# Performance work log

Hardware: AMD Instinct MI355X
Metric: run time of the kernel (lower is better)

## Reference

```python
import jax, jax.numpy as jnp
import numpy as np

NUM_GRAPHS = 128
NODES_PER_GRAPH = 512
NUM_NODES = NUM_GRAPHS * NODES_PER_GRAPH
NUM_EDGES = NUM_NODES * 16
IN_DIM = 64
HID = 128
NUM_HEADS = 4
BN_EPS = 1e-5


def setup_inputs() -> dict:
    key = jax.random.key(0)
    ks = jax.random.split(key, 12)
    x = jax.random.normal(ks[0], (NUM_NODES, IN_DIM), dtype=jnp.float32)
    edge_index = jax.random.randint(ks[1], (2, NUM_EDGES), 0, NUM_NODES, dtype=jnp.int32)
    batch = jnp.repeat(jnp.arange(NUM_GRAPHS, dtype=jnp.int32), NODES_PER_GRAPH)
    s = 0.05
    W0 = jax.random.normal(ks[2], (IN_DIM, HID), dtype=jnp.float32) * s
    b0 = jnp.zeros((HID,), jnp.float32)
    Wh = jax.random.normal(ks[3], (3, HID, HID), dtype=jnp.float32) * s  # convs 1..3
    bh = jnp.zeros((3, HID), jnp.float32)
    bn_gamma = jnp.ones((4, HID), jnp.float32)
    bn_beta = jnp.zeros((4, HID), jnp.float32)
    bn_mean = jnp.zeros((4, HID), jnp.float32)
    bn_var = jnp.ones((4, HID), jnp.float32)
    attn_in_w = jax.random.normal(ks[4], (3 * HID, HID), dtype=jnp.float32) * s
    attn_in_b = jnp.zeros((3 * HID,), jnp.float32)
    attn_out_w = jax.random.normal(ks[5], (HID, HID), dtype=jnp.float32) * s
    attn_out_b = jnp.zeros((HID,), jnp.float32)
    return dict(x=x, W0=W0, b0=b0, Wh=Wh, bh=bh, bn_gamma=bn_gamma, bn_beta=bn_beta,
                bn_mean=bn_mean, bn_var=bn_var, attn_in_w=attn_in_w, attn_in_b=attn_in_b,
                attn_out_w=attn_out_w, attn_out_b=attn_out_b, edge_index=edge_index, batch=batch)


def _forward(x, W0, b0, Wh, bh, bn_gamma, bn_beta, bn_mean, bn_var,
             attn_in_w, attn_in_b, attn_out_w, attn_out_b, edge_index, batch):
    N = x.shape[0]
    src, dst = edge_index[0], edge_index[1]
    # GCN symmetric normalization with self-loops (PyG GCNConv)
    deg = jax.ops.segment_sum(jnp.ones_like(src, jnp.float32), dst, num_segments=N) + 1.0
    dis = jax.lax.rsqrt(deg)                      # deg^{-1/2}
    enorm = (dis[src] * dis[dst])[:, None]        # per-edge norm
    self_norm = (dis * dis)[:, None]              # self-loop norm

    def gcn(h, W, b):
        h = h @ W
        agg = jax.ops.segment_sum(h[src] * enorm, dst, num_segments=N)
        return agg + h * self_norm + b

    def bn(h, i):
        scale = bn_gamma[i] * jax.lax.rsqrt(bn_var[i] + BN_EPS)
        return (h - bn_mean[i]) * scale + bn_beta[i]  # eval-mode BN

    # dropout is identity in eval mode
    h = jax.nn.relu(bn(gcn(x, W0, b0), 0))
    h = jax.nn.relu(bn(gcn(h, Wh[0], bh[0]), 1))
    h = jax.nn.relu(bn(gcn(h, Wh[1], bh[1]), 2))
    f = jax.nn.relu(bn(gcn(h, Wh[2], bh[2]), 3))   # [N, HID]

    # per-graph self-attention (equal-size contiguous graphs -> batched MHA)
    dh = HID // NUM_HEADS
    xg = f.reshape(NUM_GRAPHS, NODES_PER_GRAPH, HID)
    qkv = xg @ attn_in_w.T + attn_in_b            # [G, n, 3H]
    q, k, v = jnp.split(qkv, 3, axis=-1)

    def heads(t):
        return t.reshape(NUM_GRAPHS, NODES_PER_GRAPH, NUM_HEADS, dh).transpose(0, 2, 1, 3)
    q, k, v = heads(q), heads(k), heads(v)
    scores = jnp.einsum('ghnd,ghmd->ghnm', q, k) / np.sqrt(dh).astype(np.float32)
    attn = jax.nn.softmax(scores, axis=-1)
    o = jnp.einsum('ghnm,ghmd->ghnd', attn, v).transpose(0, 2, 1, 3).reshape(NUM_GRAPHS, NODES_PER_GRAPH, HID)
    o = o @ attn_out_w.T + attn_out_b
    final = o.reshape(N, HID)

    # global mean pool over batch indices
    cnt = jax.ops.segment_sum(jnp.ones((N,), jnp.float32), batch, num_segments=NUM_GRAPHS)
    graph_emb = jax.ops.segment_sum(final, batch, num_segments=NUM_GRAPHS) / cnt[:, None]
    return final, graph_emb


def reference(x, W0, b0, Wh, bh, bn_gamma, bn_beta, bn_mean, bn_var,
              attn_in_w, attn_in_b, attn_out_w, attn_out_b, edge_index, batch):
    return _forward(x, W0, b0, Wh, bh, bn_gamma, bn_beta, bn_mean, bn_var,
                    attn_in_w, attn_in_b, attn_out_w, attn_out_b, edge_index, batch)
```

## Files before the change

### kernel.cpp

```cpp
#include <hip/hip_runtime.h>
#include <hip/hip_bf16.h>
#include <cstdint>
#include <cstddef>

#define N_NODES 65536
#define N_EDGES 1048576
#define N_GRAPHS 128
#define NPG 512
#define IN_DIM 64
#define HID 128
#define BN_EPS 1e-5f

typedef __attribute__((ext_vector_type(8))) short bf16x8;
typedef __attribute__((ext_vector_type(4))) float f32x4;
typedef __attribute__((ext_vector_type(8))) unsigned short u16x8;
typedef __attribute__((ext_vector_type(4))) unsigned short u16x4;

__device__ inline unsigned short f2bf(float f) {
  unsigned u = __builtin_bit_cast(unsigned, f);
  u = u + 0x7fffu + ((u >> 16) & 1u);
  return (unsigned short)(u >> 16);
}
__device__ inline float bf2f(unsigned short h) {
  unsigned u = ((unsigned)h) << 16;
  return __builtin_bit_cast(float, u);
}
__device__ inline void split_bf(float v, unsigned short& hi, unsigned short& lo) {
  hi = f2bf(v);
  lo = f2bf(v - bf2f(hi));
}
__device__ inline bf16x8 ld_bf8(const unsigned short* p) {
  u16x4 a = *(const u16x4*)p;
  u16x4 b = *(const u16x4*)(p + 4);
  u16x8 r = __builtin_shufflevector(a, b, 0, 1, 2, 3, 4, 5, 6, 7);
  return __builtin_bit_cast(bf16x8, r);
}

__global__ __launch_bounds__(256) void hist_kernel(const int* __restrict__ dst,
                                                   int* __restrict__ deg) {
  int e = blockIdx.x * 256 + threadIdx.x;
  if (e < N_EDGES) atomicAdd(&deg[dst[e]], 1);
}

__global__ __launch_bounds__(256) void dis_kernel(const int* __restrict__ deg,
                                                  float* __restrict__ dis) {
  int n = blockIdx.x * 256 + threadIdx.x;
  if (n < N_NODES) dis[n] = 1.0f / sqrtf((float)deg[n] + 1.0f);
}

__global__ __launch_bounds__(1024) void scan_kernel(const int* __restrict__ deg,
                                                    int* __restrict__ offsets,
                                                    int* __restrict__ cursor) {
  __shared__ int sums[1024];
  int t = threadIdx.x;
  int base = t * 64;
  const int4* dp = (const int4*)(deg + base);
  int s = 0;
#pragma unroll
  for (int i = 0; i < 16; i++) {
    int4 v = dp[i];
    s += v.x + v.y + v.z + v.w;
  }
  sums[t] = s;
  __syncthreads();
  for (int off = 1; off < 1024; off <<= 1) {
    int v = (t >= off) ? sums[t - off] : 0;
    __syncthreads();
    sums[t] += v;
    __syncthreads();
  }
  int run = (t == 0) ? 0 : sums[t - 1];
#pragma unroll
  for (int i = 0; i < 16; i++) {
    int4 v = dp[i];
    int idx = base + i * 4;
    offsets[idx] = run; cursor[idx] = run; run += v.x;
    offsets[idx + 1] = run; cursor[idx + 1] = run; run += v.y;
    offsets[idx + 2] = run; cursor[idx + 2] = run; run += v.z;
    offsets[idx + 3] = run; cursor[idx + 3] = run; run += v.w;
  }
  if (t == 1023) offsets[N_NODES] = run;
}

__global__ __launch_bounds__(256) void fill_kernel(const int* __restrict__ src,
                                                   const int* __restrict__ dst,
                                                   const float* __restrict__ dis,
                                                   int* __restrict__ cursor,
                                                   int* __restrict__ csr,
                                                   float* __restrict__ wedge) {
  int e = blockIdx.x * 256 + threadIdx.x;
  if (e < N_EDGES) {
    int d = dst[e];
    int s = src[e];
    int slot = atomicAdd(&cursor[d], 1);
    csr[slot] = s;
    wedge[slot] = dis[s] * dis[d];
  }
}

__global__ __launch_bounds__(256) void agg64_kernel(const float* __restrict__ x,
                                                    const float* __restrict__ dis,
                                                    const float* __restrict__ wedge,
                                                    const int* __restrict__ offsets,
                                                    const int* __restrict__ csr,
                                                    unsigned short* __restrict__ zhi,
                                                    unsigned short* __restrict__ zlo) {
  int node = blockIdx.x * 4 + (threadIdx.x >> 6);
  int lane = threadIdx.x & 63;
  float dn = dis[node];
  float acc = x[(size_t)node * 64 + lane] * dn * dn;
  int beg = offsets[node], end = offsets[node + 1];
  int k = beg;
  for (; k + 8 <= end; k += 8) {
    int s[8];
    float w[8], v[8];
#pragma unroll
    for (int i = 0; i < 8; i++) {
      s[i] = csr[k + i];
      w[i] = wedge[k + i];
    }
#pragma unroll
    for (int i = 0; i < 8; i++) v[i] = x[(size_t)s[i] * 64 + lane];
#pragma unroll
    for (int i = 0; i < 8; i++) acc = fmaf(w[i], v[i], acc);
  }
  for (; k + 4 <= end; k += 4) {
    int s0 = csr[k], s1 = csr[k + 1], s2 = csr[k + 2], s3 = csr[k + 3];
    float w0 = wedge[k], w1 = wedge[k + 1], w2 = wedge[k + 2], w3 = wedge[k + 3];
    float v0 = x[(size_t)s0 * 64 + lane];
    float v1 = x[(size_t)s1 * 64 + lane];
    float v2 = x[(size_t)s2 * 64 + lane];
    float v3 = x[(size_t)s3 * 64 + lane];
    acc = fmaf(w0, v0, acc);
    acc = fmaf(w1, v1, acc);
    acc = fmaf(w2, v2, acc);
    acc = fmaf(w3, v3, acc);
  }
  for (; k < end; k++) {
    int s = csr[k];
    acc = fmaf(wedge[k], x[(size_t)s * 64 + lane], acc);
  }
  unsigned short h_, l_;
  split_bf(acc, h_, l_);
  zhi[(size_t)node * 64 + lane] = h_;
  zlo[(size_t)node * 64 + lane] = l_;
}

__global__ __launch_bounds__(256) void agg128_kernel(const float* __restrict__ h,
                                                     const float* __restrict__ dis,
                                                     const float* __restrict__ wedge,
                                                     const int* __restrict__ offsets,
                                                     const int* __restrict__ csr,
                                                     unsigned short* __restrict__ zhi,
                                                     unsigned short* __restrict__ zlo) {
  int node = blockIdx.x * 4 + (threadIdx.x >> 6);
  int lane = threadIdx.x & 63;
  float dn = dis[node];
  float sn = dn * dn;
  const float* hr = h + (size_t)node * 128;
  float a0 = hr[lane] * sn;
  float a1 = hr[lane + 64] * sn;
  int beg = offsets[node], end = offsets[node + 1];
  int k = beg;
  for (; k + 8 <= end; k += 8) {
    int s[8];
    float w[8], u[8], d[8];
#pragma unroll
    for (int i = 0; i < 8; i++) {
      s[i] = csr[k + i];
      w[i] = wedge[k + i];
    }
#pragma unroll
    for (int i = 0; i < 8; i++) {
      const float* p = h + (size_t)s[i] * 128;
      u[i] = p[lane];
      d[i] = p[lane + 64];
    }
#pragma unroll
    for (int i = 0; i < 8; i++) {
      a0 = fmaf(w[i], u[i], a0);
      a1 = fmaf(w[i], d[i], a1);
    }
  }
  for (; k + 4 <= end; k += 4) {
    int s0 = csr[k], s1 = csr[k + 1], s2 = csr[k + 2], s3 = csr[k + 3];
    float w0 = wedge[k], w1 = wedge[k + 1], w2 = wedge[k + 2], w3 = wedge[k + 3];
    const float* p0 = h + (size_t)s0 * 128;
    const float* p1 = h + (size_t)s1 * 128;
    const float* p2 = h + (size_t)s2 * 128;
    const float* p3 = h + (size_t)s3 * 128;
    float u0 = p0[lane], d0 = p0[lane + 64];
    float u1 = p1[lane], d1 = p1[lane + 64];
    float u2 = p2[lane], d2 = p2[lane + 64];
    float u3 = p3[lane], d3 = p3[lane + 64];
    a0 = fmaf(w0, u0, a0); a1 = fmaf(w0, d0, a1);
    a0 = fmaf(w1, u1, a0); a1 = fmaf(w1, d1, a1);
    a0 = fmaf(w2, u2, a0); a1 = fmaf(w2, d2, a1);
    a0 = fmaf(w3, u3, a0); a1 = fmaf(w3, d3, a1);
  }
  for (; k < end; k++) {
    int s = csr[k];
    float wt = wedge[k];
    const float* hs = h + (size_t)s * 128;
    a0 = fmaf(wt, hs[lane], a0);
    a1 = fmaf(wt, hs[lane + 64], a1);
  }
  unsigned short h0, l0, h1, l1;
  split_bf(a0, h0, l0);
  split_bf(a1, h1, l1);
  zhi[(size_t)node * 128 + lane] = h0;
  zlo[(size_t)node * 128 + lane] = l0;
  zhi[(size_t)node * 128 + lane + 64] = h1;
  zlo[(size_t)node * 128 + lane + 64] = l1;
}

template <bool TRANS>
__global__ __launch_bounds__(256) void wprep_kernel(const float* __restrict__ W, int K, int O,
                                                    unsigned short* __restrict__ hi,
                                                    unsigned short* __restrict__ lo) {
  int idx = blockIdx.x * 256 + threadIdx.x;
  int KC = K / 32;
  int total = (O / 16) * KC * 64;
  if (idx >= total) return;
  int lane = idx & 63;
  int rest = idx >> 6;
  int kc = rest % KC;
  int nt = rest / KC;
  int n = nt * 16 + (lane & 15);
  int kb = kc * 32 + (lane >> 4) * 8;
  unsigned short* hp = hi + (size_t)idx * 8;
  unsigned short* lp = lo + (size_t)idx * 8;
#pragma unroll
  for (int j = 0; j < 8; j++) {
    int k = kb + j;
    float v = TRANS ? W[(size_t)n * K + k] : W[(size_t)k * O + n];
    unsigned short h_, l_;
    split_bf(v, h_, l_);
    hp[j] = h_;
    lp[j] = l_;
  }
}

template <int K, int O, bool DOBN, bool DORELU, bool SPLIT_OUT>
__global__ __launch_bounds__(256) void gemm_mfma(
    const unsigned short* __restrict__ Ahi, const unsigned short* __restrict__ Alo,
    const unsigned short* __restrict__ Whi, const unsigned short* __restrict__ Wlo,
    const float* __restrict__ bias,
    const float* __restrict__ gamma, const float* __restrict__ beta,
    const float* __restrict__ mean, const float* __restrict__ var,
    float* __restrict__ Cf, unsigned short* __restrict__ Chi,
    unsigned short* __restrict__ Clo) {
  constexpr int KC = K / 32;
  int wave = threadIdx.x >> 6;
  int lane = threadIdx.x & 63;
  int m0 = blockIdx.x * 128 + wave * 32;
  int o0 = blockIdx.y * 128;
  int mrow = lane & 15;
  int kseg = (lane >> 4) * 8;

  f32x4 acc[2][8];
#pragma unroll
  for (int mt = 0; mt < 2; mt++)
#pragma unroll
    for (int nt = 0; nt < 8; nt++) acc[mt][nt] = (f32x4)0.0f;

#pragma unroll
  for (int kc = 0; kc < KC; kc++) {
    bf16x8 ah[2], al[2];
#pragma unroll
    for (int mt = 0; mt < 2; mt++) {
      size_t aoff = (size_t)(m0 + mt * 16 + mrow) * K + kc * 32 + kseg;
      ah[mt] = *(const bf16x8*)(Ahi + aoff);
      al[mt] = *(const bf16x8*)(Alo + aoff);
    }
#pragma unroll
    for (int nt = 0; nt < 8; nt++) {
      size_t foff = (((size_t)(blockIdx.y * 8 + nt) * KC + kc) * 64 + lane) * 8;
      bf16x8 bh = *(const bf16x8*)(Whi + foff);
      bf16x8 bl = *(const bf16x8*)(Wlo + foff);
#pragma unroll
      for (int mt = 0; mt < 2; mt++) {
        acc[mt][nt] = __builtin_amdgcn_mfma_f32_16x16x32_bf16(ah[mt], bh, acc[mt][nt], 0, 0, 0);
        acc[mt][nt] = __builtin_amdgcn_mfma_f32_16x16x32_bf16(ah[mt], bl, acc[mt][nt], 0, 0, 0);
        acc[mt][nt] = __builtin_amdgcn_mfma_f32_16x16x32_bf16(al[mt], bh, acc[mt][nt], 0, 0, 0);
      }
    }
  }

  int ccol = lane & 15;
  int crow0 = (lane >> 4) * 4;
#pragma unroll
  for (int nt = 0; nt < 8; nt++) {
    int c = o0 + nt * 16 + ccol;
    float sc, cb;
    float b = bias[c];
    if (DOBN) {
      sc = gamma[c] * rsqrtf(var[c] + BN_EPS);
      cb = (b - mean[c]) * sc + beta[c];
    } else {
      sc = 1.0f;
      cb = b;
    }
#pragma unroll
    for (int mt = 0; mt < 2; mt++) {
#pragma unroll
      for (int r = 0; r < 4; r++) {
        float v = fmaf(acc[mt][nt][r], sc, cb);
        if (DORELU) v = fmaxf(v, 0.0f);
        size_t row = (size_t)(m0 + mt * 16 + crow0 + r);
        if (SPLIT_OUT) {
          unsigned short h_, l_;
          split_bf(v, h_, l_);
          Chi[row * O + c] = h_;
          Clo[row * O + c] = l_;
        } else {
          Cf[row * O + c] = v;
        }
      }
    }
  }
}

__global__ __launch_bounds__(256) void knorm_kernel(const float* __restrict__ qkv,
                                                    float* __restrict__ kmax2) {
  int g = blockIdx.x >> 2;
  int h = blockIdx.x & 3;
  size_t gbase = (size_t)g * NPG;
  float best = 0.0f;
#pragma unroll
  for (int r = 0; r < 2; r++) {
    int j = r * 256 + threadIdx.x;
    const float* kp = &qkv[(gbase + j) * 384 + 128 + h * 32];
    float s = 0.0f;
#pragma unroll
    for (int i = 0; i < 8; i++) {
      float4 v = *(const float4*)(kp + i * 4);
      s = fmaf(v.x, v.x, s);
      s = fmaf(v.y, v.y, s);
      s = fmaf(v.z, v.z, s);
      s = fmaf(v.w, v.w, s);
    }
    best = fmaxf(best, s);
  }
#pragma unroll
  for (int off = 32; off >= 1; off >>= 1)
    best = fmaxf(best, __shfl_xor(best, off, 64));
  __shared__ float red[4];
  int wave = threadIdx.x >> 6;
  if ((threadIdx.x & 63) == 0) red[wave] = best;
  __syncthreads();
  if (threadIdx.x == 0) {
    float m = fmaxf(fmaxf(red[0], red[1]), fmaxf(red[2], red[3]));
    kmax2[blockIdx.x] = m;
  }
}

__global__ __launch_bounds__(256, 2) void attn_mfma_kernel(
    const float* __restrict__ qkv, const float* __restrict__ kmax2,
    unsigned short* __restrict__ ohi, unsigned short* __restrict__ olo) {
  int b = blockIdx.x;
  int g = b >> 3;
  int h = (b >> 1) & 3;
  int half = b & 1;
  int t = threadIdx.x;
  int wave = t >> 6;
  int lane = t & 63;
  int quad = lane >> 4;
  int l15 = lane & 15;
  size_t gbase = (size_t)g * NPG;
  int qb = half * 256 + wave * 64;

  const float cf = 0.17677669529663687f * 1.4426950408889634f;

  __shared__ unsigned short Kh[32][36], Kl[32][36];
  __shared__ unsigned short Vh[33][36], Vl[33][36];
  __shared__ char wbuf[4][9472] __attribute__((aligned(16)));

  unsigned short* Ph = (unsigned short*)wbuf[wave];
  unsigned short* Pl = Ph + 64 * 36;
  float* Ot = (float*)wbuf[wave];

  bf16x8 qh[4], ql[4];
  float qn2p[4];
#pragma unroll
  for (int mt = 0; mt < 4; mt++) {
    const float* qp = &qkv[(gbase + qb + mt * 16 + l15) * 384 + h * 32 + quad * 8];
    float4 f0 = *(const float4*)qp;
    float4 f1 = *(const float4*)(qp + 4);
    float v[8] = {f0.x * cf, f0.y * cf, f0.z * cf, f0.w * cf,
                  f1.x * cf, f1.y * cf, f1.z * cf, f1.w * cf};
    u16x8 hh, ll;
    float s = 0.0f;
#pragma unroll
    for (int j = 0; j < 8; j++) {
      unsigned short hi_, lo_;
      split_bf(v[j], hi_, lo_);
      hh[j] = hi_;
      ll[j] = lo_;
      s = fmaf(v[j], v[j], s);
    }
    qh[mt] = __builtin_bit_cast(bf16x8, hh);
    ql[mt] = __builtin_bit_cast(bf16x8, ll);
    s += __shfl_xor(s, 16);
    s += __shfl_xor(s, 32);
    qn2p[mt] = s;
  }
  if (quad == 0) {
#pragma unroll
    for (int mt = 0; mt < 4; mt++) Ot[mt * 16 + l15] = qn2p[mt];
  }
  float km2 = kmax2[g * 4 + h];
  float Mq[4][4];
#pragma unroll
  for (int mt = 0; mt < 4; mt++)
#pragma unroll
    for (int r = 0; r < 4; r++)
      Mq[mt][r] = sqrtf(Ot[mt * 16 + quad * 4 + r] * km2);

  f32x4 Oa[4][3];
#pragma unroll
  for (int mt = 0; mt < 4; mt++)
#pragma unroll
    for (int nt = 0; nt < 3; nt++) Oa[mt][nt] = (f32x4)0.0f;

  for (int c = 0; c < 16; c++) {
    __syncthreads();
    if (t >= 128) {
      int t2 = t - 128;
      int key = t2 >> 2;
      int ds = (t2 & 3) * 8;
      const float* kp = &qkv[(gbase + (size_t)(c * 32 + key)) * 384 + 128 + h * 32 + ds];
      float4 f0 = *(const float4*)kp;
      float4 f1 = *(const float4*)(kp + 4);
      float v[8] = {f0.x, f0.y, f0.z, f0.w, f1.x, f1.y, f1.z, f1.w};
      u16x4 h0, h1, l0, l1;
#pragma unroll
      for (int j = 0; j < 4; j++) {
        unsigned short hi_, lo_;
        split_bf(v[j], hi_, lo_);
        h0[j] = hi_; l0[j] = lo_;
        split_bf(v[j + 4], hi_, lo_);
        h1[j] = hi_; l1[j] = lo_;
      }
      *(u16x4*)&Kh[key][ds] = h0;
      *(u16x4*)&Kh[key][ds + 4] = h1;
      *(u16x4*)&Kl[key][ds] = l0;
      *(u16x4*)&Kl[key][ds + 4] = l1;
    } else if (t < 64) {
      int keyb = (t & 7) * 4;
      int dvb = (t >> 3) * 4;
      float4 r0 = *(const float4*)&qkv[(gbase + (size_t)(c * 32 + keyb + 0)) * 384 + 256 + h * 32 + dvb];
      float4 r1 = *(const float4*)&qkv[(gbase + (size_t)(c * 32 + keyb + 1)) * 384 + 256 + h * 32 + dvb];
      float4 r2 = *(const float4*)&qkv[(gbase + (size_t)(c * 32 + keyb + 2)) * 384 + 256 + h * 32 + dvb];
      float4 r3 = *(const float4*)&qkv[(gbase + (size_t)(c * 32 + keyb + 3)) * 384 + 256 + h * 32 + dvb];
      float rr[4][4] = {{r0.x, r0.y, r0.z, r0.w}, {r1.x, r1.y, r1.z, r1.w},
                        {r2.x, r2.y, r2.z, r2.w}, {r3.x, r3.y, r3.z, r3.w}};
#pragma unroll
      for (int c2 = 0; c2 < 4; c2++) {
        ushort4 hv, lv;
        unsigned short hi_, lo_;
        split_bf(rr[0][c2], hi_, lo_); hv.x = hi_; lv.x = lo_;
        split_bf(rr[1][c2], hi_, lo_); hv.y = hi_; lv.y = lo_;
        split_bf(rr[2][c2], hi_, lo_); hv.z = hi_; lv.z = lo_;
        split_bf(rr[3][c2], hi_, lo_); hv.w = hi_; lv.w = lo_;
        *(ushort4*)&Vh[dvb + c2][keyb] = hv;
        *(ushort4*)&Vl[dvb + c2][keyb] = lv;
      }
    } else if (t < 68) {
      int i = t - 64;
      u16x8 ones;
#pragma unroll
      for (int j = 0; j < 8; j++) ones[j] = 0x3F80;
      *(u16x4*)&Vh[32][i * 8] = __builtin_shufflevector(ones, ones, 0, 1, 2, 3);
      *(u16x4*)&Vh[32][i * 8 + 4] = __builtin_shufflevector(ones, ones, 4, 5, 6, 7);
    }
    __syncthreads();

#pragma unroll
    for (int nt = 0; nt < 2; nt++) {
      bf16x8 bkh = ld_bf8(&Kh[nt * 16 + l15][quad * 8]);
      bf16x8 bkl = ld_bf8(&Kl[nt * 16 + l15][quad * 8]);
#pragma unroll
      for (int mt = 0; mt < 4; mt++) {
        f32x4 S = (f32x4)0.0f;
        S = __builtin_amdgcn_mfma_f32_16x16x32_bf16(qh[mt], bkh, S, 0, 0, 0);
        S = __builtin_amdgcn_mfma_f32_16x16x32_bf16(qh[mt], bkl, S, 0, 0, 0);
        S = __builtin_amdgcn_mfma_f32_16x16x32_bf16(ql[mt], bkh, S, 0, 0, 0);
#pragma unroll
        for (int r = 0; r < 4; r++) {
          float p = __builtin_exp2f(S[r] - Mq[mt][r]);
          unsigned short hi_, lo_;
          split_bf(p, hi_, lo_);
          int row = mt * 16 + quad * 4 + r;
          Ph[row * 36 + nt * 16 + l15] = hi_;
          Pl[row * 36 + nt * 16 + l15] = lo_;
        }
      }
    }
    bf16x8 pah[4], pal[4];
#pragma unroll
    for (int mt = 0; mt < 4; mt++) {
      pah[mt] = ld_bf8(&Ph[(mt * 16 + l15) * 36 + quad * 8]);
      pal[mt] = ld_bf8(&Pl[(mt * 16 + l15) * 36 + quad * 8]);
    }
#pragma unroll
    for (int nt = 0; nt < 3; nt++) {
      bf16x8 bvh = ld_bf8(&Vh[nt * 16 + l15][quad * 8]);
      if (nt < 2) {
        bf16x8 bvl = ld_bf8(&Vl[nt * 16 + l15][quad * 8]);
#pragma unroll
        for (int mt = 0; mt < 4; mt++) {
          Oa[mt][nt] = __builtin_amdgcn_mfma_f32_16x16x32_bf16(pah[mt], bvh, Oa[mt][nt], 0, 0, 0);
          Oa[mt][nt] = __builtin_amdgcn_mfma_f32_16x16x32_bf16(pah[mt], bvl, Oa[mt][nt], 0, 0, 0);
          Oa[mt][nt] = __builtin_amdgcn_mfma_f32_16x16x32_bf16(pal[mt], bvh, Oa[mt][nt], 0, 0, 0);
        }
      } else {
#pragma unroll
        for (int mt = 0; mt < 4; mt++) {
          Oa[mt][nt] = __builtin_amdgcn_mfma_f32_16x16x32_bf16(pah[mt], bvh, Oa[mt][nt], 0, 0, 0);
          Oa[mt][nt] = __builtin_amdgcn_mfma_f32_16x16x32_bf16(pal[mt], bvh, Oa[mt][nt], 0, 0, 0);
        }
      }
    }
  }

#pragma unroll
  for (int mt = 0; mt < 4; mt++) {
#pragma unroll
    for (int r = 0; r < 4; r++) {
      int row = mt * 16 + quad * 4 + r;
      Ot[row * 37 + l15] = Oa[mt][0][r];
      Ot[row * 37 + 16 + l15] = Oa[mt][1][r];
      if (l15 == 0) Ot[row * 37 + 32] = Oa[mt][2][r];
    }
  }
  {
    int row = lane;
    float inv = 1.0f / Ot[row * 37 + 32];
    size_t node = gbase + qb + row;
    u16x8 vh, vl;
#pragma unroll
    for (int seg = 0; seg < 4; seg++) {
#pragma unroll
      for (int j = 0; j < 8; j++) {
        unsigned short hi_, lo_;
        split_bf(Ot[row * 37 + seg * 8 + j] * inv, hi_, lo_);
        vh[j] = hi_;
        vl[j] = lo_;
      }
      *(u16x8*)(ohi + node * 128 + h * 32 + seg * 8) = vh;
      *(u16x8*)(olo + node * 128 + h * 32 + seg * 8) = vl;
    }
  }
}

__global__ __launch_bounds__(128) void pool_kernel(const float* __restrict__ fin,
                                                   float* __restrict__ emb) {
  int g = blockIdx.x, c = threadIdx.x;
  const float* p = fin + (size_t)g * NPG * HID + c;
  float s = 0.0f;
  for (int i = 0; i < NPG; i++) s += p[(size_t)i * HID];
  emb[g * HID + c] = s * (1.0f / NPG);
}

extern "C" void kernel_launch(void* const* d_in, const int* in_sizes, int n_in,
                              void* d_out, int out_size, void* d_ws, size_t ws_size,
                              hipStream_t stream) {
  (void)in_sizes; (void)n_in; (void)out_size; (void)ws_size;
  const float* x          = (const float*)d_in[0];
  const float* W0         = (const float*)d_in[1];
  const float* b0         = (const float*)d_in[2];
  const float* Wh         = (const float*)d_in[3];
  const float* bh         = (const float*)d_in[4];
  const float* bn_gamma   = (const float*)d_in[5];
  const float* bn_beta    = (const float*)d_in[6];
  const float* bn_mean    = (const float*)d_in[7];
  const float* bn_var     = (const float*)d_in[8];
  const float* attn_in_w  = (const float*)d_in[9];
  const float* attn_in_b  = (const float*)d_in[10];
  const float* attn_out_w = (const float*)d_in[11];
  const float* attn_out_b = (const float*)d_in[12];
  const int* edge_index   = (const int*)d_in[13];
  const int* src = edge_index;
  const int* dst = edge_index + N_EDGES;

  char* ws = (char*)d_ws;
  size_t off = 0;
  auto alloc = [&](size_t bytes) -> void* {
    void* p = ws + off;
    off += (bytes + 255) & ~(size_t)255;
    return p;
  };
  int*   deg     = (int*)alloc((size_t)N_NODES * 4);
  int*   offsets = (int*)alloc((size_t)(N_NODES + 1) * 4);
  int*   cursor  = (int*)alloc((size_t)N_NODES * 4);
  int*   csr     = (int*)alloc((size_t)N_EDGES * 4);
  float* wedge   = (float*)alloc((size_t)N_EDGES * 4);
  float* dis     = (float*)alloc((size_t)N_NODES * 4);
  float* bufA    = (float*)alloc((size_t)N_NODES * HID * 4);
  unsigned short* zhi = (unsigned short*)alloc((size_t)N_NODES * HID * 2);
  unsigned short* zlo = (unsigned short*)alloc((size_t)N_NODES * HID * 2);
  float* qkvb    = (float*)alloc((size_t)N_NODES * 384 * 4);
  float* kmax2   = (float*)alloc((size_t)N_GRAPHS * 4 * 4);
  unsigned short* w0h = (unsigned short*)alloc(8192 * 2);
  unsigned short* w0l = (unsigned short*)alloc(8192 * 2);
  unsigned short* whh[3], *whl[3];
  for (int i = 0; i < 3; i++) {
    whh[i] = (unsigned short*)alloc(16384 * 2);
    whl[i] = (unsigned short*)alloc(16384 * 2);
  }
  unsigned short* wqh = (unsigned short*)alloc(49152 * 2);
  unsigned short* wql = (unsigned short*)alloc(49152 * 2);
  unsigned short* woh = (unsigned short*)alloc(16384 * 2);
  unsigned short* wol = (unsigned short*)alloc(16384 * 2);

  unsigned short* fhi = (unsigned short*)bufA;
  unsigned short* flo = fhi + (size_t)N_NODES * HID;

  float* fin = (float*)d_out;
  float* emb = fin + (size_t)N_NODES * HID;

  hipMemsetAsync(deg, 0, (size_t)N_NODES * 4, stream);
  hist_kernel<<<N_EDGES / 256, 256, 0, stream>>>(dst, deg);
  dis_kernel<<<N_NODES / 256, 256, 0, stream>>>(deg, dis);
  scan_kernel<<<1, 1024, 0, stream>>>(deg, offsets, cursor);
  fill_kernel<<<N_EDGES / 256, 256, 0, stream>>>(src, dst, dis, cursor, csr, wedge);

  wprep_kernel<false><<<4, 256, 0, stream>>>(W0, 64, 128, w0h, w0l);
  for (int i = 0; i < 3; i++)
    wprep_kernel<false><<<8, 256, 0, stream>>>(Wh + (size_t)i * HID * HID, 128, 128,
                                               whh[i], whl[i]);
  wprep_kernel<true><<<24, 256, 0, stream>>>(attn_in_w, 128, 384, wqh, wql);
  wprep_kernel<true><<<8, 256, 0, stream>>>(attn_out_w, 128, 128, woh, wol);

  dim3 ggrid(N_NODES / 128, 1);
  agg64_kernel<<<N_NODES / 4, 256, 0, stream>>>(x, dis, wedge, offsets, csr, zhi, zlo);
  gemm_mfma<64, 128, true, true, false><<<ggrid, 256, 0, stream>>>(
      zhi, zlo, w0h, w0l, b0, bn_gamma, bn_beta, bn_mean, bn_var, bufA, nullptr, nullptr);
  for (int L = 0; L < 2; L++) {
    agg128_kernel<<<N_NODES / 4, 256, 0, stream>>>(bufA, dis, wedge, offsets, csr, zhi, zlo);
    gemm_mfma<128, 128, true, true, false><<<ggrid, 256, 0, stream>>>(
        zhi, zlo, whh[L], whl[L], bh + (size_t)L * HID,
        bn_gamma + (size_t)(L + 1) * HID, bn_beta + (size_t)(L + 1) * HID,
        bn_mean + (size_t)(L + 1) * HID, bn_var + (size_t)(L + 1) * HID,
        bufA, nullptr, nullptr);
  }
  agg128_kernel<<<N_NODES / 4, 256, 0, stream>>>(bufA, dis, wedge, offsets, csr, zhi, zlo);
  gemm_mfma<128, 128, true, true, true><<<ggrid, 256, 0, stream>>>(
      zhi, zlo, whh[2], whl[2], bh + (size_t)2 * HID,
      bn_gamma + (size_t)3 * HID, bn_beta + (size_t)3 * HID,
      bn_mean + (size_t)3 * HID, bn_var + (size_t)3 * HID,
      nullptr, fhi, flo);
  dim3 qgrid(N_NODES / 128, 3);
  gemm_mfma<128, 384, false, false, false><<<qgrid, 256, 0, stream>>>(
      fhi, flo, wqh, wql, attn_in_b, nullptr, nullptr, nullptr, nullptr,
      qkvb, nullptr, nullptr);
  knorm_kernel<<<N_GRAPHS * 4, 256, 0, stream>>>(qkvb, kmax2);
  attn_mfma_kernel<<<N_GRAPHS * 4 * 2, 256, 0, stream>>>(qkvb, kmax2, zhi, zlo);
  gemm_mfma<128, 128, false, false, false><<<ggrid, 256, 0, stream>>>(
      zhi, zlo, woh, wol, attn_out_b, nullptr, nullptr, nullptr, nullptr,
      fin, nullptr, nullptr);
  pool_kernel<<<N_GRAPHS, 128, 0, stream>>>(fin, emb);
}
```

Before: 841.9 us.

## Store node features in 16-column slabs to make sparse aggregation cache-friendly

```diff
diff --git a/kernel.cpp b/kernel.cpp
--- a/kernel.cpp
+++ b/kernel.cpp
@@ -98,120 +98,65 @@
   }
 }
 
-__global__ __launch_bounds__(256) void agg64_kernel(const float* __restrict__ x,
-                                                    const float* __restrict__ dis,
-                                                    const float* __restrict__ wedge,
-                                                    const int* __restrict__ offsets,
-                                                    const int* __restrict__ csr,
-                                                    unsigned short* __restrict__ zhi,
-                                                    unsigned short* __restrict__ zlo) {
+__global__ __launch_bounds__(256) void xslab_kernel(const float* __restrict__ x,
+                                                    float* __restrict__ xs) {
   int node = blockIdx.x * 4 + (threadIdx.x >> 6);
   int lane = threadIdx.x & 63;
-  float dn = dis[node];
-  float acc = x[(size_t)node * 64 + lane] * dn * dn;
-  int beg = offsets[node], end = offsets[node + 1];
-  int k = beg;
-  for (; k + 8 <= end; k += 8) {
-    int s[8];
-    float w[8], v[8];
-#pragma unroll
-    for (int i = 0; i < 8; i++) {
-      s[i] = csr[k + i];
-      w[i] = wedge[k + i];
-    }
-#pragma unroll
-    for (int i = 0; i < 8; i++) v[i] = x[(size_t)s[i] * 64 + lane];
-#pragma unroll
-    for (int i = 0; i < 8; i++) acc = fmaf(w[i], v[i], acc);
-  }
-  for (; k + 4 <= end; k += 4) {
-    int s0 = csr[k], s1 = csr[k + 1], s2 = csr[k + 2], s3 = csr[k + 3];
-    float w0 = wedge[k], w1 = wedge[k + 1], w2 = wedge[k + 2], w3 = wedge[k + 3];
-    float v0 = x[(size_t)s0 * 64 + lane];
-    float v1 = x[(size_t)s1 * 64 + lane];
-    float v2 = x[(size_t)s2 * 64 + lane];
-    float v3 = x[(size_t)s3 * 64 + lane];
-    acc = fmaf(w0, v0, acc);
-    acc = fmaf(w1, v1, acc);
-    acc = fmaf(w2, v2, acc);
-    acc = fmaf(w3, v3, acc);
-  }
-  for (; k < end; k++) {
-    int s = csr[k];
-    acc = fmaf(wedge[k], x[(size_t)s * 64 + lane], acc);
-  }
-  unsigned short h_, l_;
-  split_bf(acc, h_, l_);
-  zhi[(size_t)node * 64 + lane] = h_;
-  zlo[(size_t)node * 64 + lane] = l_;
-}
-
-__global__ __launch_bounds__(256) void agg128_kernel(const float* __restrict__ h,
-                                                     const float* __restrict__ dis,
-                                                     const float* __restrict__ wedge,
-                                                     const int* __restrict__ offsets,
-                                                     const int* __restrict__ csr,
-                                                     unsigned short* __restrict__ zhi,
-                                                     unsigned short* __restrict__ zlo) {
-  int node = blockIdx.x * 4 + (threadIdx.x >> 6);
+  int s = lane >> 4, d = lane & 15;
+  xs[((size_t)s * N_NODES + node) * 16 + d] = x[(size_t)node * 64 + lane];
+}
+
+template <int NS>
+__global__ __launch_bounds__(256) void agg_slab_kernel(
+    const float* __restrict__ hs, const float* __restrict__ dis,
+    const float* __restrict__ wedge, const int* __restrict__ offsets,
+    const int* __restrict__ csr, unsigned short* __restrict__ zhi,
+    unsigned short* __restrict__ zlo) {
+  int b = blockIdx.x;
+  int s = b & (NS - 1);
+  int grp = b / NS;
+  int w = threadIdx.x >> 6;
   int lane = threadIdx.x & 63;
-  float dn = dis[node];
-  float sn = dn * dn;
-  const float* hr = h + (size_t)node * 128;
-  float a0 = hr[lane] * sn;
-  float a1 = hr[lane + 64] * sn;
-  int beg = offsets[node], end = offsets[node + 1];
-  int k = beg;
-  for (; k + 8 <= end; k += 8) {
-    int s[8];
-    float w[8], u[8], d[8];
-#pragma unroll
-    for (int i = 0; i < 8; i++) {
-      s[i] = csr[k + i];
-      w[i] = wedge[k + i];
-    }
-#pragma unroll
-    for (int i = 0; i < 8; i++) {
-      const float* p = h + (size_t)s[i] * 128;
-      u[i] = p[lane];
-      d[i] = p[lane + 64];
-    }
-#pragma unroll
-    for (int i = 0; i < 8; i++) {
-      a0 = fmaf(w[i], u[i], a0);
-      a1 = fmaf(w[i], d[i], a1);
-    }
-  }
-  for (; k + 4 <= end; k += 4) {
-    int s0 = csr[k], s1 = csr[k + 1], s2 = csr[k + 2], s3 = csr[k + 3];
-    float w0 = wedge[k], w1 = wedge[k + 1], w2 = wedge[k + 2], w3 = wedge[k + 3];
-    const float* p0 = h + (size_t)s0 * 128;
-    const float* p1 = h + (size_t)s1 * 128;
-    const float* p2 = h + (size_t)s2 * 128;
-    const float* p3 = h + (size_t)s3 * 128;
-    float u0 = p0[lane], d0 = p0[lane + 64];
-    float u1 = p1[lane], d1 = p1[lane + 64];
-    float u2 = p2[lane], d2 = p2[lane + 64];
-    float u3 = p3[lane], d3 = p3[lane + 64];
-    a0 = fmaf(w0, u0, a0); a1 = fmaf(w0, d0, a1);
-    a0 = fmaf(w1, u1, a0); a1 = fmaf(w1, d1, a1);
-    a0 = fmaf(w2, u2, a0); a1 = fmaf(w2, d2, a1);
-    a0 = fmaf(w3, u3, a0); a1 = fmaf(w3, d3, a1);
-  }
-  for (; k < end; k++) {
-    int s = csr[k];
-    float wt = wedge[k];
-    const float* hs = h + (size_t)s * 128;
-    a0 = fmaf(wt, hs[lane], a0);
-    a1 = fmaf(wt, hs[lane + 64], a1);
-  }
-  unsigned short h0, l0, h1, l1;
-  split_bf(a0, h0, l0);
-  split_bf(a1, h1, l1);
-  zhi[(size_t)node * 128 + lane] = h0;
-  zlo[(size_t)node * 128 + lane] = l0;
-  zhi[(size_t)node * 128 + lane + 64] = h1;
-  zlo[(size_t)node * 128 + lane + 64] = l1;
+  int e = lane >> 4, d = lane & 15;
+  const float* slab = hs + (size_t)s * N_NODES * 16;
+  const int OD = NS * 16;
+#pragma unroll 1
+  for (int i = 0; i < 4; i++) {
+    int node = (grp * 4 + w) * 4 + i;
+    int beg = offsets[node], end = offsets[node + 1];
+    float acc = 0.0f;
+    int k = beg;
+    for (; k + 8 <= end; k += 8) {
+      int i0 = csr[k + e], i1 = csr[k + 4 + e];
+      float w0 = wedge[k + e], w1 = wedge[k + 4 + e];
+      float v0 = slab[(size_t)i0 * 16 + d];
+      float v1 = slab[(size_t)i1 * 16 + d];
+      acc = fmaf(w0, v0, acc);
+      acc = fmaf(w1, v1, acc);
+    }
+    if (k + 4 <= end) {
+      int i0 = csr[k + e];
+      float w0 = wedge[k + e];
+      acc = fmaf(w0, slab[(size_t)i0 * 16 + d], acc);
+      k += 4;
+    }
+    int rem = end - k;
+    if (rem > 0) {
+      int i0 = (e < rem) ? csr[k + e] : 0;
+      float w0 = (e < rem) ? wedge[k + e] : 0.0f;
+      acc = fmaf(w0, slab[(size_t)i0 * 16 + d], acc);
+    }
+    acc += __shfl_xor(acc, 16);
+    acc += __shfl_xor(acc, 32);
+    if (e == 0) {
+      float dn = dis[node];
+      float v = fmaf(slab[(size_t)node * 16 + d], dn * dn, acc);
+      unsigned short h_, l_;
+      split_bf(v, h_, l_);
+      zhi[(size_t)node * OD + s * 16 + d] = h_;
+      zlo[(size_t)node * OD + s * 16 + d] = l_;
+    }
+  }
 }
 
 template <bool TRANS>
@@ -241,7 +186,7 @@
   }
 }
 
-template <int K, int O, bool DOBN, bool DORELU, bool SPLIT_OUT>
+template <int K, int O, bool DOBN, bool DORELU, int OUTMODE>
 __global__ __launch_bounds__(256) void gemm_mfma(
     const unsigned short* __restrict__ Ahi, const unsigned short* __restrict__ Alo,
     const unsigned short* __restrict__ Whi, const unsigned short* __restrict__ Wlo,
@@ -308,11 +253,13 @@
         float v = fmaf(acc[mt][nt][r], sc, cb);
         if (DORELU) v = fmaxf(v, 0.0f);
         size_t row = (size_t)(m0 + mt * 16 + crow0 + r);
-        if (SPLIT_OUT) {
+        if (OUTMODE == 1) {
           unsigned short h_, l_;
           split_bf(v, h_, l_);
           Chi[row * O + c] = h_;
           Clo[row * O + c] = l_;
+        } else if (OUTMODE == 2) {
+          Cf[((size_t)(c >> 4) * N_NODES + row) * 16 + (c & 15)] = v;
         } else {
           Cf[row * O + c] = v;
         }
@@ -597,7 +544,8 @@
   int*   csr     = (int*)alloc((size_t)N_EDGES * 4);
   float* wedge   = (float*)alloc((size_t)N_EDGES * 4);
   float* dis     = (float*)alloc((size_t)N_NODES * 4);
-  float* bufA    = (float*)alloc((size_t)N_NODES * HID * 4);
+  float* hsl     = (float*)alloc((size_t)N_NODES * HID * 4);
+  float* xs      = (float*)alloc((size_t)N_NODES * 64 * 4);
   unsigned short* zhi = (unsigned short*)alloc((size_t)N_NODES * HID * 2);
   unsigned short* zlo = (unsigned short*)alloc((size_t)N_NODES * HID * 2);
   float* qkvb    = (float*)alloc((size_t)N_NODES * 384 * 4);
@@ -614,7 +562,7 @@
   unsigned short* woh = (unsigned short*)alloc(16384 * 2);
   unsigned short* wol = (unsigned short*)alloc(16384 * 2);
 
-  unsigned short* fhi = (unsigned short*)bufA;
+  unsigned short* fhi = (unsigned short*)hsl;
   unsigned short* flo = fhi + (size_t)N_NODES * HID;
 
   float* fin = (float*)d_out;
@@ -633,31 +581,36 @@
   wprep_kernel<true><<<24, 256, 0, stream>>>(attn_in_w, 128, 384, wqh, wql);
   wprep_kernel<true><<<8, 256, 0, stream>>>(attn_out_w, 128, 128, woh, wol);
 
+  xslab_kernel<<<N_NODES / 4, 256, 0, stream>>>(x, xs);
+
   dim3 ggrid(N_NODES / 128, 1);
-  agg64_kernel<<<N_NODES / 4, 256, 0, stream>>>(x, dis, wedge, offsets, csr, zhi, zlo);
-  gemm_mfma<64, 128, true, true, false><<<ggrid, 256, 0, stream>>>(
-      zhi, zlo, w0h, w0l, b0, bn_gamma, bn_beta, bn_mean, bn_var, bufA, nullptr, nullptr);
+  agg_slab_kernel<4><<<(N_NODES / 16) * 4, 256, 0, stream>>>(
+      xs, dis, wedge, offsets, csr, zhi, zlo);
+  gemm_mfma<64, 128, true, true, 2><<<ggrid, 256, 0, stream>>>(
+      zhi, zlo, w0h, w0l, b0, bn_gamma, bn_beta, bn_mean, bn_var, hsl, nullptr, nullptr);
   for (int L = 0; L < 2; L++) {
-    agg128_kernel<<<N_NODES / 4, 256, 0, stream>>>(bufA, dis, wedge, offsets, csr, zhi, zlo);
-    gemm_mfma<128, 128, true, true, false><<<ggrid, 256, 0, stream>>>(
+    agg_slab_kernel<8><<<(N_NODES / 16) * 8, 256, 0, stream>>>(
+        hsl, dis, wedge, offsets, csr, zhi, zlo);
+    gemm_mfma<128, 128, true, true, 2><<<ggrid, 256, 0, stream>>>(
         zhi, zlo, whh[L], whl[L], bh + (size_t)L * HID,
         bn_gamma + (size_t)(L + 1) * HID, bn_beta + (size_t)(L + 1) * HID,
         bn_mean + (size_t)(L + 1) * HID, bn_var + (size_t)(L + 1) * HID,
-        bufA, nullptr, nullptr);
-  }
-  agg128_kernel<<<N_NODES / 4, 256, 0, stream>>>(bufA, dis, wedge, offsets, csr, zhi, zlo);
-  gemm_mfma<128, 128, true, true, true><<<ggrid, 256, 0, stream>>>(
+        hsl, nullptr, nullptr);
+  }
+  agg_slab_kernel<8><<<(N_NODES / 16) * 8, 256, 0, stream>>>(
+      hsl, dis, wedge, offsets, csr, zhi, zlo);
+  gemm_mfma<128, 128, true, true, 1><<<ggrid, 256, 0, stream>>>(
       zhi, zlo, whh[2], whl[2], bh + (size_t)2 * HID,
       bn_gamma + (size_t)3 * HID, bn_beta + (size_t)3 * HID,
       bn_mean + (size_t)3 * HID, bn_var + (size_t)3 * HID,
       nullptr, fhi, flo);
   dim3 qgrid(N_NODES / 128, 3);
-  gemm_mfma<128, 384, false, false, false><<<qgrid, 256, 0, stream>>>(
+  gemm_mfma<128, 384, false, false, 0><<<qgrid, 256, 0, stream>>>(
       fhi, flo, wqh, wql, attn_in_b, nullptr, nullptr, nullptr, nullptr,
       qkvb, nullptr, nullptr);
   knorm_kernel<<<N_GRAPHS * 4, 256, 0, stream>>>(qkvb, kmax2);
   attn_mfma_kernel<<<N_GRAPHS * 4 * 2, 256, 0, stream>>>(qkvb, kmax2, zhi, zlo);
-  gemm_mfma<128, 128, false, false, false><<<ggrid, 256, 0, stream>>>(
+  gemm_mfma<128, 128, false, false, 0><<<ggrid, 256, 0, stream>>>(
       zhi, zlo, woh, wol, attn_out_b, nullptr, nullptr, nullptr, nullptr,
       fin, nullptr, nullptr);
   pool_kernel<<<N_GRAPHS, 128, 0, stream>>>(fin, emb);
```

Result: slower. 1.230 ms (+46.1%).

## Fuse GCN neighbor aggregation into the MFMA GEMM with an LDS-staged tile

Applied to the files above, without the earlier changes.

```diff
diff --git a/kernel.cpp b/kernel.cpp
--- a/kernel.cpp
+++ b/kernel.cpp
@@ -96,122 +96,6 @@
     csr[slot] = s;
     wedge[slot] = dis[s] * dis[d];
   }
-}
-
-__global__ __launch_bounds__(256) void agg64_kernel(const float* __restrict__ x,
-                                                    const float* __restrict__ dis,
-                                                    const float* __restrict__ wedge,
-                                                    const int* __restrict__ offsets,
-                                                    const int* __restrict__ csr,
-                                                    unsigned short* __restrict__ zhi,
-                                                    unsigned short* __restrict__ zlo) {
-  int node = blockIdx.x * 4 + (threadIdx.x >> 6);
-  int lane = threadIdx.x & 63;
-  float dn = dis[node];
-  float acc = x[(size_t)node * 64 + lane] * dn * dn;
-  int beg = offsets[node], end = offsets[node + 1];
-  int k = beg;
-  for (; k + 8 <= end; k += 8) {
-    int s[8];
-    float w[8], v[8];
-#pragma unroll
-    for (int i = 0; i < 8; i++) {
-      s[i] = csr[k + i];
-      w[i] = wedge[k + i];
-    }
-#pragma unroll
-    for (int i = 0; i < 8; i++) v[i] = x[(size_t)s[i] * 64 + lane];
-#pragma unroll
-    for (int i = 0; i < 8; i++) acc = fmaf(w[i], v[i], acc);
-  }
-  for (; k + 4 <= end; k += 4) {
-    int s0 = csr[k], s1 = csr[k + 1], s2 = csr[k + 2], s3 = csr[k + 3];
-    float w0 = wedge[k], w1 = wedge[k + 1], w2 = wedge[k + 2], w3 = wedge[k + 3];
-    float v0 = x[(size_t)s0 * 64 + lane];
-    float v1 = x[(size_t)s1 * 64 + lane];
-    float v2 = x[(size_t)s2 * 64 + lane];
-    float v3 = x[(size_t)s3 * 64 + lane];
-    acc = fmaf(w0, v0, acc);
-    acc = fmaf(w1, v1, acc);
-    acc = fmaf(w2, v2, acc);
-    acc = fmaf(w3, v3, acc);
-  }
-  for (; k < end; k++) {
-    int s = csr[k];
-    acc = fmaf(wedge[k], x[(size_t)s * 64 + lane], acc);
-  }
-  unsigned short h_, l_;
-  split_bf(acc, h_, l_);
-  zhi[(size_t)node * 64 + lane] = h_;
-  zlo[(size_t)node * 64 + lane] = l_;
-}
-
-__global__ __launch_bounds__(256) void agg128_kernel(const float* __restrict__ h,
-                                                     const float* __restrict__ dis,
-                                                     const float* __restrict__ wedge,
-                                                     const int* __restrict__ offsets,
-                                                     const int* __restrict__ csr,
-                                                     unsigned short* __restrict__ zhi,
-                                                     unsigned short* __restrict__ zlo) {
-  int node = blockIdx.x * 4 + (threadIdx.x >> 6);
-  int lane = threadIdx.x & 63;
-  float dn = dis[node];
-  float sn = dn * dn;
-  const float* hr = h + (size_t)node * 128;
-  float a0 = hr[lane] * sn;
-  float a1 = hr[lane + 64] * sn;
-  int beg = offsets[node], end = offsets[node + 1];
-  int k = beg;
-  for (; k + 8 <= end; k += 8) {
-    int s[8];
-    float w[8], u[8], d[8];
-#pragma unroll
-    for (int i = 0; i < 8; i++) {
-      s[i] = csr[k + i];
-      w[i] = wedge[k + i];
-    }
-#pragma unroll
-    for (int i = 0; i < 8; i++) {
-      const float* p = h + (size_t)s[i] * 128;
-      u[i] = p[lane];
-      d[i] = p[lane + 64];
-    }
-#pragma unroll
-    for (int i = 0; i < 8; i++) {
-      a0 = fmaf(w[i], u[i], a0);
-      a1 = fmaf(w[i], d[i], a1);
-    }
-  }
-  for (; k + 4 <= end; k += 4) {
-    int s0 = csr[k], s1 = csr[k + 1], s2 = csr[k + 2], s3 = csr[k + 3];
-    float w0 = wedge[k], w1 = wedge[k + 1], w2 = wedge[k + 2], w3 = wedge[k + 3];
-    const float* p0 = h + (size_t)s0 * 128;
-    const float* p1 = h + (size_t)s1 * 128;
-    const float* p2 = h + (size_t)s2 * 128;
-    const float* p3 = h + (size_t)s3 * 128;
-    float u0 = p0[lane], d0 = p0[lane + 64];
-    float u1 = p1[lane], d1 = p1[lane + 64];
-    float u2 = p2[lane], d2 = p2[lane + 64];
-    float u3 = p3[lane], d3 = p3[lane + 64];
-    a0 = fmaf(w0, u0, a0); a1 = fmaf(w0, d0, a1);
-    a0 = fmaf(w1, u1, a0); a1 = fmaf(w1, d1, a1);
-    a0 = fmaf(w2, u2, a0); a1 = fmaf(w2, d2, a1);
-    a0 = fmaf(w3, u3, a0); a1 = fmaf(w3, d3, a1);
-  }
-  for (; k < end; k++) {
-    int s = csr[k];
-    float wt = wedge[k];
-    const float* hs = h + (size_t)s * 128;
-    a0 = fmaf(wt, hs[lane], a0);
-    a1 = fmaf(wt, hs[lane + 64], a1);
-  }
-  unsigned short h0, l0, h1, l1;
-  split_bf(a0, h0, l0);
-  split_bf(a1, h1, l1);
-  zhi[(size_t)node * 128 + lane] = h0;
-  zlo[(size_t)node * 128 + lane] = l0;
-  zhi[(size_t)node * 128 + lane + 64] = h1;
-  zlo[(size_t)node * 128 + lane + 64] = l1;
 }
 
 template <bool TRANS>
@@ -241,7 +125,160 @@
   }
 }
 
-template <int K, int O, bool DOBN, bool DORELU, bool SPLIT_OUT>
+template <int K, int OUTMODE>
+__global__ __launch_bounds__(256, 2) void fused_agg_gemm(
+    const float* __restrict__ h, const float* __restrict__ dis,
+    const float* __restrict__ wedge, const int* __restrict__ offsets,
+    const int* __restrict__ csr,
+    const unsigned short* __restrict__ Whi, const unsigned short* __restrict__ Wlo,
+    const float* __restrict__ bias,
+    const float* __restrict__ gamma, const float* __restrict__ beta,
+    const float* __restrict__ mean, const float* __restrict__ var,
+    float* __restrict__ Cf, unsigned short* __restrict__ Chi,
+    unsigned short* __restrict__ Clo) {
+  constexpr int KC = K / 32;
+  constexpr int O = 128;
+  int wave = threadIdx.x >> 6;
+  int lane = threadIdx.x & 63;
+  int quad = lane >> 4;
+  int l15 = lane & 15;
+  int m0 = blockIdx.x * 128;
+  int base = m0 + wave * 32;
+
+  __shared__ unsigned short Zh[4][32][K], Zl[4][32][K];
+
+  int go = lane & 7;
+  int gl = lane >> 3;
+  for (int r = 0; r < 32; r++) {
+    int node = base + r;
+    float dn = dis[node];
+    float sn = dn * dn;
+    int beg = offsets[node], end = offsets[node + 1];
+    float a0, a1 = 0.0f;
+    if (K == 64) {
+      a0 = h[(size_t)node * 64 + lane] * sn;
+    } else {
+      const float* hr = h + (size_t)node * 128;
+      a0 = hr[lane] * sn;
+      a1 = hr[lane + 64] * sn;
+    }
+    int k = beg;
+    for (; k + 8 <= end; k += 8) {
+      int s[8];
+      float w[8], u[8], d[8];
+#pragma unroll
+      for (int i = 0; i < 8; i++) {
+        s[i] = csr[k + i];
+        w[i] = wedge[k + i];
+      }
+      if (K == 64) {
+#pragma unroll
+        for (int i = 0; i < 8; i++) u[i] = h[(size_t)s[i] * 64 + lane];
+#pragma unroll
+        for (int i = 0; i < 8; i++) a0 = fmaf(w[i], u[i], a0);
+      } else {
+#pragma unroll
+        for (int i = 0; i < 8; i++) {
+          const float* p = h + (size_t)s[i] * 128;
+          u[i] = p[lane];
+          d[i] = p[lane + 64];
+        }
+#pragma unroll
+        for (int i = 0; i < 8; i++) {
+          a0 = fmaf(w[i], u[i], a0);
+          a1 = fmaf(w[i], d[i], a1);
+        }
+      }
+    }
+    for (; k < end; k++) {
+      int s = csr[k];
+      float wt = wedge[k];
+      if (K == 64) {
+        a0 = fmaf(wt, h[(size_t)s * 64 + lane], a0);
+      } else {
+        const float* hs = h + (size_t)s * 128;
+        a0 = fmaf(wt, hs[lane], a0);
+        a1 = fmaf(wt, hs[lane + 64], a1);
+      }
+    }
+    int rx = r & 7;
+    int gs = (gl ^ rx) & 7;
+    unsigned short h0, l0;
+    split_bf(a0, h0, l0);
+    int d0 = (gs << 3) | go;
+    Zh[wave][r][d0] = h0;
+    Zl[wave][r][d0] = l0;
+    if (K == 128) {
+      unsigned short h1, l1;
+      split_bf(a1, h1, l1);
+      int d1 = ((8 | gs) << 3) | go;
+      Zh[wave][r][d1] = h1;
+      Zl[wave][r][d1] = l1;
+    }
+  }
+  __syncthreads();
+
+  f32x4 acc[2][8];
+#pragma unroll
+  for (int mt = 0; mt < 2; mt++)
+#pragma unroll
+    for (int nt = 0; nt < 8; nt++) acc[mt][nt] = (f32x4)0.0f;
+
+#pragma unroll
+  for (int kc = 0; kc < KC; kc++) {
+    bf16x8 ah[2], al[2];
+#pragma unroll
+    for (int mt = 0; mt < 2; mt++) {
+      int r = mt * 16 + l15;
+      int rx = r & 7;
+      int g = kc * 4 + quad;
+      int gp = (g & 8) | ((g ^ rx) & 7);
+      ah[mt] = ld_bf8(&Zh[wave][r][gp * 8]);
+      al[mt] = ld_bf8(&Zl[wave][r][gp * 8]);
+    }
+#pragma unroll
+    for (int nt = 0; nt < 8; nt++) {
+      size_t foff = (((size_t)nt * KC + kc) * 64 + lane) * 8;
+      bf16x8 bh = *(const bf16x8*)(Whi + foff);
+      bf16x8 bl = *(const bf16x8*)(Wlo + foff);
+#pragma unroll
+      for (int mt = 0; mt < 2; mt++) {
+        acc[mt][nt] = __builtin_amdgcn_mfma_f32_16x16x32_bf16(ah[mt], bh, acc[mt][nt], 0, 0, 0);
+        acc[mt][nt] = __builtin_amdgcn_mfma_f32_16x16x32_bf16(ah[mt], bl, acc[mt][nt], 0, 0, 0);
+        acc[mt][nt] = __builtin_amdgcn_mfma_f32_16x16x32_bf16(al[mt], bh, acc[mt][nt], 0, 0, 0);
+      }
+    }
+  }
+
+  int ccol = l15;
+  int crow0 = quad * 4;
+#pragma unroll
+  for (int nt = 0; nt < 8; nt++) {
+    int c = nt * 16 + ccol;
+    float b = bias[c];
+    float sc = gamma[c] * rsqrtf(var[c] + BN_EPS);
+    float cb = (b - mean[c]) * sc + beta[c];
+#pragma unroll
+    for (int mt = 0; mt < 2; mt++) {
+#pragma unroll
+      for (int r = 0; r < 4; r++) {
+        float v = fmaf(acc[mt][nt][r], sc, cb);
+        v = fmaxf(v, 0.0f);
+        size_t row = (size_t)(m0 + wave * 32 + mt * 16 + crow0 + r);
+        if (OUTMODE == 1) {
+          unsigned short h_, l_;
+          split_bf(v, h_, l_);
+          Chi[row * O + c] = h_;
+          Clo[row * O + c] = l_;
+        } else {
+          Cf[row * O + c] = v;
+        }
+      }
+    }
+  }
+}
+
+template <int K, int O, bool DOBN, bool DORELU, int OUTMODE>
 __global__ __launch_bounds__(256) void gemm_mfma(
     const unsigned short* __restrict__ Ahi, const unsigned short* __restrict__ Alo,
     const unsigned short* __restrict__ Whi, const unsigned short* __restrict__ Wlo,
@@ -308,7 +345,7 @@
         float v = fmaf(acc[mt][nt][r], sc, cb);
         if (DORELU) v = fmaxf(v, 0.0f);
         size_t row = (size_t)(m0 + mt * 16 + crow0 + r);
-        if (SPLIT_OUT) {
+        if (OUTMODE == 1) {
           unsigned short h_, l_;
           split_bf(v, h_, l_);
           Chi[row * O + c] = h_;
@@ -598,6 +635,7 @@
   float* wedge   = (float*)alloc((size_t)N_EDGES * 4);
   float* dis     = (float*)alloc((size_t)N_NODES * 4);
   float* bufA    = (float*)alloc((size_t)N_NODES * HID * 4);
+  float* bufB    = (float*)alloc((size_t)N_NODES * HID * 4);
   unsigned short* zhi = (unsigned short*)alloc((size_t)N_NODES * HID * 2);
   unsigned short* zlo = (unsigned short*)alloc((size_t)N_NODES * HID * 2);
   float* qkvb    = (float*)alloc((size_t)N_NODES * 384 * 4);
@@ -614,7 +652,7 @@
   unsigned short* woh = (unsigned short*)alloc(16384 * 2);
   unsigned short* wol = (unsigned short*)alloc(16384 * 2);
 
-  unsigned short* fhi = (unsigned short*)bufA;
+  unsigned short* fhi = (unsigned short*)bufB;
   unsigned short* flo = fhi + (size_t)N_NODES * HID;
 
   float* fin = (float*)d_out;
@@ -633,31 +671,28 @@
   wprep_kernel<true><<<24, 256, 0, stream>>>(attn_in_w, 128, 384, wqh, wql);
   wprep_kernel<true><<<8, 256, 0, stream>>>(attn_out_w, 128, 128, woh, wol);
 
-  dim3 ggrid(N_NODES / 128, 1);
-  agg64_kernel<<<N_NODES / 4, 256, 0, stream>>>(x, dis, wedge, offsets, csr, zhi, zlo);
-  gemm_mfma<64, 128, true, true, false><<<ggrid, 256, 0, stream>>>(
-      zhi, zlo, w0h, w0l, b0, bn_gamma, bn_beta, bn_mean, bn_var, bufA, nullptr, nullptr);
-  for (int L = 0; L < 2; L++) {
-    agg128_kernel<<<N_NODES / 4, 256, 0, stream>>>(bufA, dis, wedge, offsets, csr, zhi, zlo);
-    gemm_mfma<128, 128, true, true, false><<<ggrid, 256, 0, stream>>>(
-        zhi, zlo, whh[L], whl[L], bh + (size_t)L * HID,
-        bn_gamma + (size_t)(L + 1) * HID, bn_beta + (size_t)(L + 1) * HID,
-        bn_mean + (size_t)(L + 1) * HID, bn_var + (size_t)(L + 1) * HID,
-        bufA, nullptr, nullptr);
-  }
-  agg128_kernel<<<N_NODES / 4, 256, 0, stream>>>(bufA, dis, wedge, offsets, csr, zhi, zlo);
-  gemm_mfma<128, 128, true, true, true><<<ggrid, 256, 0, stream>>>(
-      zhi, zlo, whh[2], whl[2], bh + (size_t)2 * HID,
-      bn_gamma + (size_t)3 * HID, bn_beta + (size_t)3 * HID,
-      bn_mean + (size_t)3 * HID, bn_var + (size_t)3 * HID,
+  dim3 fgrid(N_NODES / 128, 1);
+  fused_agg_gemm<64, 0><<<fgrid, 256, 0, stream>>>(
+      x, dis, wedge, offsets, csr, w0h, w0l, b0,
+      bn_gamma, bn_beta, bn_mean, bn_var, bufA, nullptr, nullptr);
+  fused_agg_gemm<128, 0><<<fgrid, 256, 0, stream>>>(
+      bufA, dis, wedge, offsets, csr, whh[0], whl[0], bh,
+      bn_gamma + HID, bn_beta + HID, bn_mean + HID, bn_var + HID, bufB, nullptr, nullptr);
+  fused_agg_gemm<128, 0><<<fgrid, 256, 0, stream>>>(
+      bufB, dis, wedge, offsets, csr, whh[1], whl[1], bh + HID,
+      bn_gamma + 2 * HID, bn_beta + 2 * HID, bn_mean + 2 * HID, bn_var + 2 * HID,
+      bufA, nullptr, nullptr);
+  fused_agg_gemm<128, 1><<<fgrid, 256, 0, stream>>>(
+      bufA, dis, wedge, offsets, csr, whh[2], whl[2], bh + 2 * HID,
+      bn_gamma + 3 * HID, bn_beta + 3 * HID, bn_mean + 3 * HID, bn_var + 3 * HID,
       nullptr, fhi, flo);
   dim3 qgrid(N_NODES / 128, 3);
-  gemm_mfma<128, 384, false, false, false><<<qgrid, 256, 0, stream>>>(
+  gemm_mfma<128, 384, false, false, 0><<<qgrid, 256, 0, stream>>>(
       fhi, flo, wqh, wql, attn_in_b, nullptr, nullptr, nullptr, nullptr,
       qkvb, nullptr, nullptr);
   knorm_kernel<<<N_GRAPHS * 4, 256, 0, stream>>>(qkvb, kmax2);
   attn_mfma_kernel<<<N_GRAPHS * 4 * 2, 256, 0, stream>>>(qkvb, kmax2, zhi, zlo);
-  gemm_mfma<128, 128, false, false, false><<<ggrid, 256, 0, stream>>>(
+  gemm_mfma<128, 128, false, false, 0><<<fgrid, 256, 0, stream>>>(
       zhi, zlo, woh, wol, attn_out_b, nullptr, nullptr, nullptr, nullptr,
       fin, nullptr, nullptr);
   pool_kernel<<<N_GRAPHS, 128, 0, stream>>>(fin, emb);
```

Result: slower. 1.008 ms (+19.7%).
